# Optimization experiments

Measured on AMD Instinct MI355X. Metric: run time of the kernel, lower is better.

## Reference

```python
import jax, jax.numpy as jnp
import numpy as np

N_NODES = 100000
N_EDGES = 500000
D = 256
EPS = 0.1  # GIN epsilon applied on self-loop relation


def setup_inputs() -> dict:
    key = jax.random.key(0)
    ks = jax.random.split(key, 9)
    return {
        "x": jax.random.normal(ks[0], (N_NODES, D), dtype=jnp.float32),
        "W_self": jax.random.normal(ks[1], (D, D), dtype=jnp.float32) * 0.05,
        "W_r1": jax.random.normal(ks[2], (D, D), dtype=jnp.float32) * 0.05,
        "W_r2": jax.random.normal(ks[3], (D, D), dtype=jnp.float32) * 0.05,
        "bias": jax.random.normal(ks[4], (D,), dtype=jnp.float32) * 0.05,
        "src1": jax.random.randint(ks[5], (N_EDGES,), 0, N_NODES, dtype=jnp.int32),
        "dst1": jax.random.randint(ks[6], (N_EDGES,), 0, N_NODES, dtype=jnp.int32),
        "src2": jax.random.randint(ks[7], (N_EDGES,), 0, N_NODES, dtype=jnp.int32),
        "dst2": jax.random.randint(ks[8], (N_EDGES,), 0, N_NODES, dtype=jnp.int32),
    }


def reference(x, W_self, W_r1, W_r2, bias, src1, dst1, src2, dst2):
    # self-loop relation: features scaled by (1+eps); one self-loop edge per node
    # so copy_u + sum delivers each node exactly its own message.
    h = (1.0 + EPS) * (x @ W_self)
    # regular relations: per-node message = x @ W, gathered along src edges,
    # scatter-summed at dst (DGL fn.copy_u + fn.sum, cross-etype 'sum' reducer).
    msg1 = x @ W_r1
    h = h + jax.ops.segment_sum(msg1[src1], dst1, num_segments=N_NODES)
    msg2 = x @ W_r2
    h = h + jax.ops.segment_sum(msg2[src2], dst2, num_segments=N_NODES)
    # bias + activation, then second activation (applied twice in original);
    # mlp/batch_norm are None, dropout is identity in eval.
    h = jax.nn.relu(h + bias)
    h = jax.nn.relu(h)
    return h
```

## Files before the change

### kernel.cpp

```cpp
#include <hip/hip_runtime.h>

#define N_NODES 100000
#define N_EDGES 500000
#define D 256
#define CAP 32
#define BM 128

typedef __bf16 bf16x8 __attribute__((ext_vector_type(8)));
typedef float  f32x4  __attribute__((ext_vector_type(4)));
typedef unsigned int u32x2 __attribute__((ext_vector_type(2)));

__device__ __forceinline__ unsigned short f2bf(float f) {
    unsigned int u = __float_as_uint(f);
    u += 0x7fffu + ((u >> 16) & 1u);
    return (unsigned short)(u >> 16);
}
__device__ __forceinline__ float bf2f(unsigned short b) {
    return __uint_as_float(((unsigned int)b) << 16);
}

__device__ __forceinline__ void glds16(const unsigned short* g, unsigned short* l) {
    __builtin_amdgcn_global_load_lds(
        (const __attribute__((address_space(1))) unsigned int*)g,
        (__attribute__((address_space(3))) unsigned int*)l,
        16, 0, 0);
}

#define PREP_BLOCKS 17188

__global__ __launch_bounds__(256) void prep_kernel(
    const float* __restrict__ x, unsigned short* __restrict__ xb,
    const float* __restrict__ Ws, const float* __restrict__ W1,
    const float* __restrict__ W2, unsigned short* __restrict__ Wt,
    const int* __restrict__ src1, const int* __restrict__ dst1,
    const int* __restrict__ src2, const int* __restrict__ dst2,
    int* __restrict__ cnt1, int* __restrict__ cnt2,
    int* __restrict__ bkt1, int* __restrict__ bkt2)
{
    const int wid  = blockIdx.x * 4 + (threadIdx.x >> 6);
    const int lane = threadIdx.x & 63;
    const int group = wid / 22;
    const int pos   = wid - group * 22;

    if (pos < 16) {
        int cw = group * 16 + pos;
        if (cw >= 50000) return;
        size_t base = (size_t)cw * 512;
        float4 a = *(const float4*)(x + base + lane * 4);
        float4 c = *(const float4*)(x + base + 256 + lane * 4);
        ushort4 oa, oc;
        oa.x = f2bf(a.x); oa.y = f2bf(a.y); oa.z = f2bf(a.z); oa.w = f2bf(a.w);
        oc.x = f2bf(c.x); oc.y = f2bf(c.y); oc.z = f2bf(c.z); oc.w = f2bf(c.w);
        *(ushort4*)(xb + base + lane * 4) = oa;
        *(ushort4*)(xb + base + 256 + lane * 4) = oc;
    } else if (pos < 21) {
        int bw = group * 5 + (pos - 16);
        int e = bw * 64 + lane;
        if (e >= 2 * N_EDGES) return;
        bool r2 = (e >= N_EDGES);
        const int* src = r2 ? src2 : src1;
        const int* dst = r2 ? dst2 : dst1;
        int* cnt = r2 ? cnt2 : cnt1;
        int* bkt = r2 ? bkt2 : bkt1;
        int ei = r2 ? e - N_EDGES : e;
        int s = src[ei], d = dst[ei];
        int p = atomicAdd(&cnt[d], 1);
        if (p < CAP) bkt[d * CAP + p] = s;
    } else {
        int idx = group * 64 + lane;
        if (idx >= 3 * D * D) return;
        int k = idx >> 8;
        int n = idx & (D - 1);
        const float* W = (k < D) ? Ws : (k < 2 * D ? W1 : W2);
        float scale = (k < D) ? 1.1f : 1.0f;
        int dk = k ^ ((((n >> 1) & 3)) << 3);
        Wt[(size_t)n * (3 * D) + dk] = f2bf(W[(size_t)(k & (D - 1)) * D + n] * scale);
    }
}

__global__ __launch_bounds__(256) void gather_kernel(
    const unsigned short* __restrict__ xb,
    const int* __restrict__ cnt1, const int* __restrict__ cnt2,
    const int* __restrict__ bkt1, const int* __restrict__ bkt2,
    unsigned short* __restrict__ xa1, unsigned short* __restrict__ xa2)
{
    long long gid = (long long)blockIdx.x * blockDim.x + threadIdx.x;
    int node = (int)(gid >> 6);
    int lane = (int)(gid & 63);
    if (node >= N_NODES) return;

    int c1 = cnt1[node]; if (c1 > CAP) c1 = CAP;
    int c2 = cnt2[node]; if (c2 > CAP) c2 = CAP;
    int sid1 = (lane < c1) ? bkt1[(size_t)node * CAP + lane] : 0;
    int sid2 = (lane < c2) ? bkt2[(size_t)node * CAP + lane] : 0;

    ushort4 v1[8], v2[8];
    #pragma unroll
    for (int t = 0; t < 8; ++t)
        v1[t] = *(const ushort4*)(xb + (size_t)__shfl(sid1, t) * D + lane * 4);
    #pragma unroll
    for (int t = 0; t < 8; ++t)
        v2[t] = *(const ushort4*)(xb + (size_t)__shfl(sid2, t) * D + lane * 4);

    {
        float a0 = 0.f, a1 = 0.f, a2 = 0.f, a3 = 0.f;
        #pragma unroll
        for (int t = 0; t < 8; ++t)
            if (t < c1) {
                a0 += bf2f(v1[t].x); a1 += bf2f(v1[t].y);
                a2 += bf2f(v1[t].z); a3 += bf2f(v1[t].w);
            }
        for (int e = 8; e < c1; ++e) {
            int s = __shfl(sid1, e);
            ushort4 t = *(const ushort4*)(xb + (size_t)s * D + lane * 4);
            a0 += bf2f(t.x); a1 += bf2f(t.y); a2 += bf2f(t.z); a3 += bf2f(t.w);
        }
        u32x2 o;
        o.x = (unsigned)f2bf(a0) | ((unsigned)f2bf(a1) << 16);
        o.y = (unsigned)f2bf(a2) | ((unsigned)f2bf(a3) << 16);
        *(u32x2*)(xa1 + (size_t)node * D + lane * 4) = o;
    }

    {
        float a0 = 0.f, a1 = 0.f, a2 = 0.f, a3 = 0.f;
        #pragma unroll
        for (int t = 0; t < 8; ++t)
            if (t < c2) {
                a0 += bf2f(v2[t].x); a1 += bf2f(v2[t].y);
                a2 += bf2f(v2[t].z); a3 += bf2f(v2[t].w);
            }
        for (int e = 8; e < c2; ++e) {
            int s = __shfl(sid2, e);
            ushort4 t = *(const ushort4*)(xb + (size_t)s * D + lane * 4);
            a0 += bf2f(t.x); a1 += bf2f(t.y); a2 += bf2f(t.z); a3 += bf2f(t.w);
        }
        u32x2 o;
        o.x = (unsigned)f2bf(a0) | ((unsigned)f2bf(a1) << 16);
        o.y = (unsigned)f2bf(a2) | ((unsigned)f2bf(a3) << 16);
        *(u32x2*)(xa2 + (size_t)node * D + lane * 4) = o;
    }
}

__global__ __launch_bounds__(512, 4) void gemm_kernel(
    const unsigned short* __restrict__ xb,
    const unsigned short* __restrict__ xa1,
    const unsigned short* __restrict__ xa2,
    const unsigned short* __restrict__ Wt,
    const float* __restrict__ bias, float* __restrict__ out)
{
    __shared__ unsigned short Alds[3][BM * 32];
    __shared__ unsigned short Blds[3][256 * 32];

    const int tid  = threadIdx.x;
    const int lane = tid & 63;
    const int wave = tid >> 6;
    const int quad = lane >> 4;
    const int l15  = lane & 15;
    const int m0 = blockIdx.x * BM;
    const int wm = (wave >> 2) * 64;
    const int wn = (wave & 3) * 64;
    const int swz = (l15 >> 1) & 3;

    const int gr   = lane >> 2;
    const int gch  = lane & 3;
    const int gswz = (lane >> 3) & 3;
    int mRow = m0 + (wave << 4) + gr;
    if (mRow >= N_NODES) mRow = N_NODES - 1;
    const size_t aRowOff = (size_t)mRow * D + ((gch ^ gswz) << 3);
    const unsigned short* bSrc0 = Wt + (size_t)((wave << 4) + gr) * (3 * D) + (gch << 3);
    const unsigned short* bSrc1 = bSrc0 + (size_t)128 * (3 * D);
    const unsigned short* Aseg[3] = {xb, xa1, xa2};

    f32x4 acc[4][4] = {};

    glds16(Aseg[0] + aRowOff,            &Alds[0][wave * 512]);
    glds16(bSrc0,                        &Blds[0][wave * 512]);
    glds16(bSrc1,                        &Blds[0][4096 + wave * 512]);
    glds16(Aseg[0] + aRowOff + 32,       &Alds[1][wave * 512]);
    glds16(bSrc0 + 32,                   &Blds[1][wave * 512]);
    glds16(bSrc1 + 32,                   &Blds[1][4096 + wave * 512]);

    for (int kt = 0; kt < 24; ++kt) {
        const int kpre = kt + 2;
        if (kpre < 24) {
            const int b = kpre % 3;
            glds16(Aseg[kpre >> 3] + aRowOff + ((kpre & 7) * 32), &Alds[b][wave * 512]);
            glds16(bSrc0 + kpre * 32, &Blds[b][wave * 512]);
            glds16(bSrc1 + kpre * 32, &Blds[b][4096 + wave * 512]);
        }

        if (kt < 22)       asm volatile("s_waitcnt vmcnt(6)" ::: "memory");
        else if (kt == 22) asm volatile("s_waitcnt vmcnt(3)" ::: "memory");
        else               asm volatile("s_waitcnt vmcnt(0)" ::: "memory");
        __builtin_amdgcn_s_barrier();
        asm volatile("" ::: "memory");

        const unsigned short* Ab = &Alds[kt % 3][0];
        const unsigned short* Bb = &Blds[kt % 3][0];
        bf16x8 b0f = *(const bf16x8*)(Bb + (wn +  0 + l15) * 32 + ((quad ^ swz) * 8));
        bf16x8 b1f = *(const bf16x8*)(Bb + (wn + 16 + l15) * 32 + ((quad ^ swz) * 8));
        bf16x8 b2f = *(const bf16x8*)(Bb + (wn + 32 + l15) * 32 + ((quad ^ swz) * 8));
        bf16x8 b3f = *(const bf16x8*)(Bb + (wn + 48 + l15) * 32 + ((quad ^ swz) * 8));
        #pragma unroll
        for (int i = 0; i < 4; ++i) {
            bf16x8 afi = *(const bf16x8*)(Ab + (wm + i * 16 + l15) * 32 + ((quad ^ swz) * 8));
            acc[i][0] = __builtin_amdgcn_mfma_f32_16x16x32_bf16(afi, b0f, acc[i][0], 0, 0, 0);
            acc[i][1] = __builtin_amdgcn_mfma_f32_16x16x32_bf16(afi, b1f, acc[i][1], 0, 0, 0);
            acc[i][2] = __builtin_amdgcn_mfma_f32_16x16x32_bf16(afi, b2f, acc[i][2], 0, 0, 0);
            acc[i][3] = __builtin_amdgcn_mfma_f32_16x16x32_bf16(afi, b3f, acc[i][3], 0, 0, 0);
        }

        asm volatile("" ::: "memory");
        __builtin_amdgcn_s_barrier();
        asm volatile("" ::: "memory");
    }

    #pragma unroll
    for (int j = 0; j < 4; ++j) {
        int col = wn + j * 16 + l15;
        float bj = bias[col];
        #pragma unroll
        for (int i = 0; i < 4; ++i) {
            int rb = m0 + wm + i * 16 + quad * 4;
            #pragma unroll
            for (int r = 0; r < 4; ++r) {
                int m = rb + r;
                if (m < N_NODES)
                    __builtin_nontemporal_store(
                        fmaxf(acc[i][j][r] + bj, 0.f),
                        out + (size_t)m * D + col);
            }
        }
    }
}

extern "C" void kernel_launch(void* const* d_in, const int* in_sizes, int n_in,
                              void* d_out, int out_size, void* d_ws, size_t ws_size,
                              hipStream_t stream) {
    const float* x    = (const float*)d_in[0];
    const float* Ws   = (const float*)d_in[1];
    const float* W1   = (const float*)d_in[2];
    const float* W2   = (const float*)d_in[3];
    const float* bias = (const float*)d_in[4];
    const int* src1   = (const int*)d_in[5];
    const int* dst1   = (const int*)d_in[6];
    const int* src2   = (const int*)d_in[7];
    const int* dst2   = (const int*)d_in[8];
    float* out = (float*)d_out;

    char* p = (char*)d_ws;
    unsigned short* xb  = (unsigned short*)p; p += (size_t)N_NODES * D * 2;
    unsigned short* xa1 = (unsigned short*)p; p += (size_t)N_NODES * D * 2;
    unsigned short* xa2 = (unsigned short*)p; p += (size_t)N_NODES * D * 2;
    int* cnt1 = (int*)p; p += (size_t)N_NODES * 4;
    int* cnt2 = (int*)p; p += (size_t)N_NODES * 4;
    int* bkt1 = (int*)p; p += (size_t)N_NODES * CAP * 4;
    int* bkt2 = (int*)p; p += (size_t)N_NODES * CAP * 4;
    unsigned short* Wt = (unsigned short*)p;

    (void)hipMemsetAsync(cnt1, 0, (size_t)2 * N_NODES * 4, stream);

    prep_kernel<<<PREP_BLOCKS, 256, 0, stream>>>(
        x, xb, Ws, W1, W2, Wt, src1, dst1, src2, dst2, cnt1, cnt2, bkt1, bkt2);

    {
        long long total = (long long)N_NODES * 64;
        gather_kernel<<<(int)((total + 255) / 256), 256, 0, stream>>>(
            xb, cnt1, cnt2, bkt1, bkt2, xa1, xa2);
    }
    {
        gemm_kernel<<<(N_NODES + BM - 1) / BM, 512, 0, stream>>>(
            xb, xa1, xa2, Wt, bias, out);
    }
}
```

Measured before the change: 376.8 us.

## Interleave edge counts with buckets, add nontemporal gather stores and MFMA priority

Merges the per-node count and source bucket into one 33-int row, so the gather reads count and sources from adjacent memory and the atomic and bucket write touch the same line. Gather outputs are written with nontemporal stores, and the GEMM MFMA section raises wave priority with s_setprio. The memset now clears the whole bucket array, not just the counts, which is a much larger fill. The nontemporal stores may also evict data the GEMM rereads soon after.

```diff
diff --git a/kernel.cpp b/kernel.cpp
--- a/kernel.cpp
+++ b/kernel.cpp
@@ -4,6 +4,7 @@
 #define N_EDGES 500000
 #define D 256
 #define CAP 32
+#define BROW 33
 #define BM 128
 
 typedef __bf16 bf16x8 __attribute__((ext_vector_type(8)));
@@ -34,8 +35,7 @@
     const float* __restrict__ W2, unsigned short* __restrict__ Wt,
     const int* __restrict__ src1, const int* __restrict__ dst1,
     const int* __restrict__ src2, const int* __restrict__ dst2,
-    int* __restrict__ cnt1, int* __restrict__ cnt2,
-    int* __restrict__ bkt1, int* __restrict__ bkt2)
+    int* __restrict__ bc1, int* __restrict__ bc2)
 {
     const int wid  = blockIdx.x * 4 + (threadIdx.x >> 6);
     const int lane = threadIdx.x & 63;
@@ -60,12 +60,11 @@
         bool r2 = (e >= N_EDGES);
         const int* src = r2 ? src2 : src1;
         const int* dst = r2 ? dst2 : dst1;
-        int* cnt = r2 ? cnt2 : cnt1;
-        int* bkt = r2 ? bkt2 : bkt1;
+        int* bc = r2 ? bc2 : bc1;
         int ei = r2 ? e - N_EDGES : e;
         int s = src[ei], d = dst[ei];
-        int p = atomicAdd(&cnt[d], 1);
-        if (p < CAP) bkt[d * CAP + p] = s;
+        int p = atomicAdd(&bc[(size_t)d * BROW], 1);
+        if (p < CAP) bc[(size_t)d * BROW + 1 + p] = s;
     } else {
         int idx = group * 64 + lane;
         if (idx >= 3 * D * D) return;
@@ -80,8 +79,7 @@
 
 __global__ __launch_bounds__(256) void gather_kernel(
     const unsigned short* __restrict__ xb,
-    const int* __restrict__ cnt1, const int* __restrict__ cnt2,
-    const int* __restrict__ bkt1, const int* __restrict__ bkt2,
+    const int* __restrict__ bc1, const int* __restrict__ bc2,
     unsigned short* __restrict__ xa1, unsigned short* __restrict__ xa2)
 {
     long long gid = (long long)blockIdx.x * blockDim.x + threadIdx.x;
@@ -89,10 +87,10 @@
     int lane = (int)(gid & 63);
     if (node >= N_NODES) return;
 
-    int c1 = cnt1[node]; if (c1 > CAP) c1 = CAP;
-    int c2 = cnt2[node]; if (c2 > CAP) c2 = CAP;
-    int sid1 = (lane < c1) ? bkt1[(size_t)node * CAP + lane] : 0;
-    int sid2 = (lane < c2) ? bkt2[(size_t)node * CAP + lane] : 0;
+    int c1 = bc1[(size_t)node * BROW]; if (c1 > CAP) c1 = CAP;
+    int c2 = bc2[(size_t)node * BROW]; if (c2 > CAP) c2 = CAP;
+    int sid1 = (lane < c1) ? bc1[(size_t)node * BROW + 1 + lane] : 0;
+    int sid2 = (lane < c2) ? bc2[(size_t)node * BROW + 1 + lane] : 0;
 
     ushort4 v1[8], v2[8];
     #pragma unroll
@@ -118,7 +116,7 @@
         u32x2 o;
         o.x = (unsigned)f2bf(a0) | ((unsigned)f2bf(a1) << 16);
         o.y = (unsigned)f2bf(a2) | ((unsigned)f2bf(a3) << 16);
-        *(u32x2*)(xa1 + (size_t)node * D + lane * 4) = o;
+        __builtin_nontemporal_store(o, (u32x2*)(xa1 + (size_t)node * D + lane * 4));
     }
 
     {
@@ -137,7 +135,7 @@
         u32x2 o;
         o.x = (unsigned)f2bf(a0) | ((unsigned)f2bf(a1) << 16);
         o.y = (unsigned)f2bf(a2) | ((unsigned)f2bf(a3) << 16);
-        *(u32x2*)(xa2 + (size_t)node * D + lane * 4) = o;
+        __builtin_nontemporal_store(o, (u32x2*)(xa2 + (size_t)node * D + lane * 4));
     }
 }
 
@@ -201,6 +199,7 @@
         bf16x8 b1f = *(const bf16x8*)(Bb + (wn + 16 + l15) * 32 + ((quad ^ swz) * 8));
         bf16x8 b2f = *(const bf16x8*)(Bb + (wn + 32 + l15) * 32 + ((quad ^ swz) * 8));
         bf16x8 b3f = *(const bf16x8*)(Bb + (wn + 48 + l15) * 32 + ((quad ^ swz) * 8));
+        __builtin_amdgcn_s_setprio(1);
         #pragma unroll
         for (int i = 0; i < 4; ++i) {
             bf16x8 afi = *(const bf16x8*)(Ab + (wm + i * 16 + l15) * 32 + ((quad ^ swz) * 8));
@@ -209,6 +208,7 @@
             acc[i][2] = __builtin_amdgcn_mfma_f32_16x16x32_bf16(afi, b2f, acc[i][2], 0, 0, 0);
             acc[i][3] = __builtin_amdgcn_mfma_f32_16x16x32_bf16(afi, b3f, acc[i][3], 0, 0, 0);
         }
+        __builtin_amdgcn_s_setprio(0);
 
         asm volatile("" ::: "memory");
         __builtin_amdgcn_s_barrier();
@@ -252,21 +252,19 @@
     unsigned short* xb  = (unsigned short*)p; p += (size_t)N_NODES * D * 2;
     unsigned short* xa1 = (unsigned short*)p; p += (size_t)N_NODES * D * 2;
     unsigned short* xa2 = (unsigned short*)p; p += (size_t)N_NODES * D * 2;
-    int* cnt1 = (int*)p; p += (size_t)N_NODES * 4;
-    int* cnt2 = (int*)p; p += (size_t)N_NODES * 4;
-    int* bkt1 = (int*)p; p += (size_t)N_NODES * CAP * 4;
-    int* bkt2 = (int*)p; p += (size_t)N_NODES * CAP * 4;
+    int* bc1 = (int*)p; p += (size_t)N_NODES * BROW * 4;
+    int* bc2 = (int*)p; p += (size_t)N_NODES * BROW * 4;
     unsigned short* Wt = (unsigned short*)p;
 
-    (void)hipMemsetAsync(cnt1, 0, (size_t)2 * N_NODES * 4, stream);
+    (void)hipMemsetAsync(bc1, 0, (size_t)2 * N_NODES * BROW * 4, stream);
 
     prep_kernel<<<PREP_BLOCKS, 256, 0, stream>>>(
-        x, xb, Ws, W1, W2, Wt, src1, dst1, src2, dst2, cnt1, cnt2, bkt1, bkt2);
+        x, xb, Ws, W1, W2, Wt, src1, dst1, src2, dst2, bc1, bc2);
 
     {
         long long total = (long long)N_NODES * 64;
         gather_kernel<<<(int)((total + 255) / 256), 256, 0, stream>>>(
-            xb, cnt1, cnt2, bkt1, bkt2, xa1, xa2);
+            xb, bc1, bc2, xa1, xa2);
     }
     {
         gemm_kernel<<<(N_NODES + BM - 1) / BM, 512, 0, stream>>>(
```

New measurement: 388.9 us. 1.03x slower.
